# Optimization experiments

Hardware: AMD Instinct MI355X
Metric: run time of the kernel (lower is better)

The kernel has to match this reference:

```python
import jax, jax.numpy as jnp
import numpy as np

BATCH, SEQ, D_MODEL, D_STATE = 16, 1024, 512, 32
DT_MIN, DT_MAX, DT_FLOOR = 1e-3, 1e-1, 1e-4


def _init_ssm(key):
    k1, k2, k3, k4 = jax.random.split(key, 4)
    scale = 1.0 / np.sqrt(D_STATE)
    z = jax.random.normal(k1, (D_MODEL, D_STATE)) * scale
    A_log = -jnp.exp(z)  # A = exp(A_log) in (0,1)
    B = jax.random.normal(k2, (D_MODEL, D_STATE)) * scale
    C = jax.random.normal(k3, (D_MODEL, D_STATE)) * scale
    log_dt = jax.random.uniform(k4, (D_MODEL,)) * (np.log(DT_MAX) - np.log(DT_MIN)) + np.log(DT_MIN)
    log_dt = jnp.maximum(log_dt, np.log(DT_FLOOR))
    return A_log, B, C, log_dt


def setup_inputs() -> dict:
    key = jax.random.key(0)
    kx, khr, kbr = jax.random.split(key, 3)
    x = jax.random.normal(kx, (BATCH, SEQ, D_MODEL), dtype=jnp.float32)
    A_log_hr, B_hr, C_hr, log_dt_hr = _init_ssm(khr)
    A_log_br, B_br, C_br, log_dt_br = _init_ssm(kbr)
    return dict(
        x=x,
        A_log_hr=A_log_hr, B_hr=B_hr, C_hr=C_hr, log_dt_hr=log_dt_hr,
        A_log_br=A_log_br, B_br=B_br, C_br=C_br, log_dt_br=log_dt_br,
        weight_hr=jnp.ones((D_MODEL,), jnp.float32),
        weight_br=jnp.ones((D_MODEL,), jnp.float32),
    )


def _ssm(x, A_log, B, C, log_dt):
    # delta=None path: dt = exp(log_dt) * dt_scale(=1), time-invariant -> dA, dB are [d, n]
    dt = jnp.exp(log_dt)                 # [d]
    A = jnp.exp(A_log)                   # [d, n]
    dA = jnp.exp(dt[:, None] * A)        # [d, n]  (matches torch: exp(dt*exp(A_log)))
    dB = dt[:, None] * B                 # [d, n]
    b = x.shape[0]
    h0 = jnp.zeros((b, A.shape[0], A.shape[1]), x.dtype)  # [b, d, n]

    def step(h, xt):  # xt: [b, d]
        h = dA * h + dB * xt[:, :, None]
        y = jnp.einsum('bdn,dn->bd', h, C)
        return h, y

    _, ys = jax.lax.scan(step, h0, jnp.swapaxes(x, 0, 1))  # ys: [L, b, d]
    return jnp.swapaxes(ys, 0, 1)        # [b, L, d]


def reference(x, A_log_hr, B_hr, C_hr, log_dt_hr,
              A_log_br, B_br, C_br, log_dt_br,
              weight_hr, weight_br):
    x_hr = _ssm(x, A_log_hr, B_hr, C_hr, log_dt_hr) * weight_hr  # [b, L, d]
    x_br = _ssm(x, A_log_br, B_br, C_br, log_dt_br) * weight_br
    return (x_hr, x_br, x_hr + x_br)  # hr_enhanced, br_enhanced, combined
```

## Files before the change

kernel.cpp:

```cpp
#include <hip/hip_runtime.h>

#define BATCH 16
#define SEQ   1024
#define DM    512
#define NST   32
#define PF    8

#define PIN(v) asm volatile("" : "+v"(v))


__global__ __launch_bounds__(256) void ssm_setup(
    const float* __restrict__ Alog_hr, const float* __restrict__ B_hr,
    const float* __restrict__ C_hr,    const float* __restrict__ ldt_hr,
    const float* __restrict__ Alog_br, const float* __restrict__ B_br,
    const float* __restrict__ C_br,    const float* __restrict__ ldt_br,
    const float* __restrict__ w_hr,    const float* __restrict__ w_br,
    float* __restrict__ dA_tbl, float* __restrict__ Cw_tbl)
{
    int idx = blockIdx.x * blockDim.x + threadIdx.x;
    int d   = idx & (DM - 1);
    int n   = (idx >> 9) & (NST - 1);
    int ssm = idx >> 14;

    const float* Alog = ssm ? Alog_br : Alog_hr;
    const float* Bm   = ssm ? B_br    : B_hr;
    const float* Cm   = ssm ? C_br    : C_hr;
    const float* ldt  = ssm ? ldt_br  : ldt_hr;
    const float* w    = ssm ? w_br    : w_hr;

    float dt = expf(ldt[d]);
    float a  = expf(Alog[d * NST + n]);
    dA_tbl[idx] = expf(dt * a);
    Cw_tbl[idx] = Cm[d * NST + n] * Bm[d * NST + n] * dt * w[d];
}

__global__ __launch_bounds__(256) void ssm_pass1(
    const float* __restrict__ x,
    const float* __restrict__ Alog_hr, const float* __restrict__ ldt_hr,
    const float* __restrict__ Alog_br, const float* __restrict__ ldt_br,
    float* __restrict__ E, int nc, int cl)
{
    int tid  = threadIdx.x;
    int dlo  = tid & 127;
    int nh   = tid >> 7;
    int bid  = blockIdx.x;
    int dblk = bid & 3;
    int r    = bid >> 2;
    int ncm1 = nc - 1;
    int c    = r % ncm1;  r /= ncm1;
    int b    = r & (BATCH - 1);
    int ssm  = r >> 4;
    int d    = dblk * 128 + dlo;
    int n0   = nh * 16;

    const float* Alog = ssm ? Alog_br : Alog_hr;
    const float* ldt  = ssm ? ldt_br  : ldt_hr;

    float dt = expf(ldt[d]);
    float dA[16], g[16];
#pragma unroll
    for (int i = 0; i < 16; ++i) {
        dA[i] = expf(dt * expf(Alog[d * NST + n0 + i]));
        g[i]  = 0.f;
    }
#pragma unroll
    for (int i = 0; i < 16; ++i) PIN(dA[i]);

    const float* xp = x + ((size_t)b * SEQ + (size_t)c * cl) * DM + d;

    float xf[PF];
#pragma unroll
    for (int k = 0; k < PF; ++k) xf[k] = xp[(size_t)k * DM];
    const float* xq = xp + (size_t)PF * DM;

    int ntb = cl / PF;
    for (int t8 = 0; t8 < ntb - 1; ++t8) {
#pragma unroll
        for (int j = 0; j < PF; ++j) {
            float xv = xf[j];
            xf[j] = xq[(size_t)j * DM];
#pragma unroll
            for (int i = 0; i < 16; ++i) g[i] = fmaf(dA[i], g[i], xv);
        }
        xq += (size_t)PF * DM;
    }
#pragma unroll
    for (int j = 0; j < PF; ++j) {
        float xv = xf[j];
#pragma unroll
        for (int i = 0; i < 16; ++i) g[i] = fmaf(dA[i], g[i], xv);
    }

    float* sp = E + ((((size_t)ssm * BATCH + b) * nc + c) * NST + n0) * DM + d;
#pragma unroll
    for (int i = 0; i < 16; ++i) sp[(size_t)i * DM] = g[i];
}

__global__ __launch_bounds__(256) void ssm_pass2(
    const float* __restrict__ Alog_hr, const float* __restrict__ B_hr,
    const float* __restrict__ C_hr,    const float* __restrict__ ldt_hr,
    const float* __restrict__ Alog_br, const float* __restrict__ B_br,
    const float* __restrict__ C_br,    const float* __restrict__ ldt_br,
    const float* __restrict__ w_hr,    const float* __restrict__ w_br,
    float* __restrict__ E,
    float* __restrict__ dA_tbl, float* __restrict__ Cw_tbl,
    int nc, int cl)
{
    int idx = blockIdx.x * blockDim.x + threadIdx.x;
    int d   = idx & (DM - 1);
    int n   = (idx >> 9) & (NST - 1);
    int b   = (idx >> 14) & 15;
    int ssm = idx >> 18;

    const float* Alog = ssm ? Alog_br : Alog_hr;
    const float* ldt  = ssm ? ldt_br  : ldt_hr;

    float dt = expf(ldt[d]);
    float A  = expf(Alog[d * NST + n]);
    float p  = expf((float)cl * dt * A);

    if (b == 0) {
        const float* Bm = ssm ? B_br : B_hr;
        const float* Cm = ssm ? C_br : C_hr;
        const float* w  = ssm ? w_br : w_hr;
        int tix = (ssm * NST + n) * DM + d;
        dA_tbl[tix] = expf(dt * A);
        Cw_tbl[tix] = Cm[d * NST + n] * Bm[d * NST + n] * dt * w[d];
    }

    float* sp = E + ((((size_t)ssm * BATCH + b) * nc) * NST + n) * DM + d;
    size_t cstride = (size_t)NST * DM;

    float H = 0.f;
    for (int c = 0; c < nc; ++c) {
        float s = *sp;
        *sp = H;
        H = fmaf(p, H, s);
        sp += cstride;
    }
}

__global__ __launch_bounds__(128, 2) void ssm_pass3(
    const float* __restrict__ x,
    const float* __restrict__ dA_tbl, const float* __restrict__ Cw_tbl,
    const float* __restrict__ E,
    float* __restrict__ out_hr, float* __restrict__ out_br, float* __restrict__ out_cb,
    int nc, int cl)
{
    int tid  = threadIdx.x;
    int lane = tid & 63;
    int wid  = tid >> 6;
    int ssm  = lane >> 5;
    int dlo  = lane & 31;
    int bid  = blockIdx.x;
    int dblk = bid & 7;
    int r    = bid >> 3;
    int c    = r % nc;
    int b    = r / nc;
    int d    = dblk * 64 + wid * 32 + dlo;

    const float* dat = dA_tbl + (size_t)ssm * NST * DM + d;
    const float* cwt = Cw_tbl + (size_t)ssm * NST * DM + d;
    float dA[NST], Cw[NST];
#pragma unroll
    for (int n = 0; n < NST; ++n) {
        dA[n] = dat[(size_t)n * DM];
        Cw[n] = cwt[(size_t)n * DM];
    }
#pragma unroll
    for (int n = 0; n < NST; ++n) { PIN(dA[n]); PIN(Cw[n]); }

    float g[NST];
    if (c == 0) {
#pragma unroll
        for (int n = 0; n < NST; ++n) g[n] = 0.f;
    } else {
        const float* sp = E + ((((size_t)ssm * BATCH + b) * nc + c) * NST) * DM + d;
#pragma unroll
        for (int n = 0; n < NST; ++n) g[n] = sp[(size_t)n * DM];
    }

    size_t off = ((size_t)b * SEQ + (size_t)c * cl) * DM + d;
    const float* xp = x + off;
    float* po = (ssm ? out_br : out_hr) + off;
    float* oc = out_cb + off;

    float xf[PF];
#pragma unroll
    for (int k = 0; k < PF; ++k) xf[k] = xp[(size_t)k * DM];
    const float* xq = xp + (size_t)PF * DM;

#define BODY8(DOPF)                                                     \
    {                                                                   \
        float xc[PF];                                                   \
        _Pragma("unroll")                                               \
        for (int j = 0; j < PF; ++j) xc[j] = xf[j];                     \
        if (DOPF) {                             \
            _Pragma("unroll")                                           \
            for (int j = 0; j < PF; ++j) xf[j] = xq[(size_t)j * DM];    \
        }                                                               \
        float yv[PF], yw[PF];                                           \
        _Pragma("unroll")                                               \
        for (int j = 0; j < PF; ++j) {                                  \
            float xv = xc[j];                                           \
            float y0 = 0.f, y1 = 0.f, y2 = 0.f, y3 = 0.f;               \
            _Pragma("unroll")                                           \
            for (int n = 0; n < NST; n += 4) {                          \
                g[n]     = fmaf(dA[n],     g[n],     xv);               \
                g[n + 1] = fmaf(dA[n + 1], g[n + 1], xv);               \
                g[n + 2] = fmaf(dA[n + 2], g[n + 2], xv);               \
                g[n + 3] = fmaf(dA[n + 3], g[n + 3], xv);               \
                y0 = fmaf(Cw[n],     g[n],     y0);                     \
                y1 = fmaf(Cw[n + 1], g[n + 1], y1);                     \
                y2 = fmaf(Cw[n + 2], g[n + 2], y2);                     \
                y3 = fmaf(Cw[n + 3], g[n + 3], y3);                     \
            }                                                           \
            float y = (y0 + y1) + (y2 + y3);                            \
            yv[j] = y;                                                  \
            yw[j] = __shfl_xor(y, 32, 64);      \
            po[(size_t)j * DM] = y;                \
        }                                                               \
        if (ssm == 0) {                           \
            _Pragma("unroll")                                           \
            for (int j = 0; j < PF; ++j)                                \
                oc[(size_t)j * DM] = yv[j] + yw[j];                     \
        }                                                               \
        po += (size_t)PF * DM;  oc += (size_t)PF * DM;                  \
    }

    int ntb = cl / PF;
    for (int t8 = 0; t8 < ntb - 1; ++t8) {
        BODY8(1);
        xq += (size_t)PF * DM;
    }
    BODY8(0);
#undef BODY8
}

extern "C" void kernel_launch(void* const* d_in, const int* in_sizes, int n_in,
                              void* d_out, int out_size, void* d_ws, size_t ws_size,
                              hipStream_t stream)
{
    (void)in_sizes; (void)n_in; (void)out_size;

    const float* x       = (const float*)d_in[0];
    const float* Alog_hr = (const float*)d_in[1];
    const float* B_hr    = (const float*)d_in[2];
    const float* C_hr    = (const float*)d_in[3];
    const float* ldt_hr  = (const float*)d_in[4];
    const float* Alog_br = (const float*)d_in[5];
    const float* B_br    = (const float*)d_in[6];
    const float* C_br    = (const float*)d_in[7];
    const float* ldt_br  = (const float*)d_in[8];
    const float* w_hr    = (const float*)d_in[9];
    const float* w_br    = (const float*)d_in[10];

    float* out    = (float*)d_out;
    const size_t one = (size_t)BATCH * SEQ * DM;
    float* out_hr = out;
    float* out_br = out + one;
    float* out_cb = out + 2 * one;

    float* dA_tbl = (float*)d_ws;
    float* Cw_tbl = dA_tbl + (size_t)2 * NST * DM;
    float* E      = Cw_tbl + (size_t)2 * NST * DM;

    const size_t tbl_bytes = (size_t)4 * NST * DM * sizeof(float);
    int nc = 8;
    while (nc > 1 &&
           ws_size < tbl_bytes + (size_t)2 * BATCH * nc * NST * DM * sizeof(float))
        nc >>= 1;
    int cl = SEQ / nc;

    if (nc > 1) {
        int nblk1 = 2 * BATCH * (nc - 1) * 4;
        ssm_pass1<<<nblk1, 256, 0, stream>>>(x, Alog_hr, ldt_hr, Alog_br, ldt_br,
                                             E, nc, cl);
        int total2 = 2 * BATCH * NST * DM;
        ssm_pass2<<<total2 / 256, 256, 0, stream>>>(Alog_hr, B_hr, C_hr, ldt_hr,
                                                    Alog_br, B_br, C_br, ldt_br,
                                                    w_hr, w_br, E, dA_tbl, Cw_tbl,
                                                    nc, cl);
    } else {
        int total0 = 2 * NST * DM;
        ssm_setup<<<total0 / 256, 256, 0, stream>>>(Alog_hr, B_hr, C_hr, ldt_hr,
                                                    Alog_br, B_br, C_br, ldt_br,
                                                    w_hr, w_br, dA_tbl, Cw_tbl);
    }

    int nblk3 = BATCH * nc * 8;
    ssm_pass3<<<nblk3, 128, 0, stream>>>(x, dA_tbl, Cw_tbl, E,
                                         out_hr, out_br, out_cb, nc, cl);
}
```

Baseline: 68.08 us.

## Split state dimension across lane halves in pass3 to double parallelism

Result: slower. 74.91 us (+10.0%).

```diff
diff --git a/kernel.cpp b/kernel.cpp
--- a/kernel.cpp
+++ b/kernel.cpp
@@ -140,7 +140,7 @@
     }
 }
 
-__global__ __launch_bounds__(128, 2) void ssm_pass3(
+__global__ __launch_bounds__(128, 4) void ssm_pass3(
     const float* __restrict__ x,
     const float* __restrict__ dA_tbl, const float* __restrict__ Cw_tbl,
     const float* __restrict__ E,
@@ -151,39 +151,40 @@
     int lane = tid & 63;
     int wid  = tid >> 6;
     int ssm  = lane >> 5;
-    int dlo  = lane & 31;
+    int nh   = (lane >> 4) & 1;
+    int dlo  = lane & 15;
     int bid  = blockIdx.x;
-    int dblk = bid & 7;
-    int r    = bid >> 3;
+    int dblk = bid & 15;
+    int r    = bid >> 4;
     int c    = r % nc;
     int b    = r / nc;
-    int d    = dblk * 64 + wid * 32 + dlo;
-
-    const float* dat = dA_tbl + (size_t)ssm * NST * DM + d;
-    const float* cwt = Cw_tbl + (size_t)ssm * NST * DM + d;
-    float dA[NST], Cw[NST];
-#pragma unroll
-    for (int n = 0; n < NST; ++n) {
+    int d    = dblk * 32 + wid * 16 + dlo;
+    int n0   = nh * 16;
+
+    const float* dat = dA_tbl + ((size_t)ssm * NST + n0) * DM + d;
+    const float* cwt = Cw_tbl + ((size_t)ssm * NST + n0) * DM + d;
+    float dA[16], Cw[16];
+#pragma unroll
+    for (int n = 0; n < 16; ++n) {
         dA[n] = dat[(size_t)n * DM];
         Cw[n] = cwt[(size_t)n * DM];
     }
 #pragma unroll
-    for (int n = 0; n < NST; ++n) { PIN(dA[n]); PIN(Cw[n]); }
-
-    float g[NST];
+    for (int n = 0; n < 16; ++n) { PIN(dA[n]); PIN(Cw[n]); }
+
+    float g[16];
     if (c == 0) {
 #pragma unroll
-        for (int n = 0; n < NST; ++n) g[n] = 0.f;
+        for (int n = 0; n < 16; ++n) g[n] = 0.f;
     } else {
-        const float* sp = E + ((((size_t)ssm * BATCH + b) * nc + c) * NST) * DM + d;
-#pragma unroll
-        for (int n = 0; n < NST; ++n) g[n] = sp[(size_t)n * DM];
+        const float* sp = E + ((((size_t)ssm * BATCH + b) * nc + c) * NST + n0) * DM + d;
+#pragma unroll
+        for (int n = 0; n < 16; ++n) g[n] = sp[(size_t)n * DM];
     }
 
     size_t off = ((size_t)b * SEQ + (size_t)c * cl) * DM + d;
     const float* xp = x + off;
-    float* po = (ssm ? out_br : out_hr) + off;
-    float* oc = out_cb + off;
+    float* po = (nh ? out_cb : (ssm ? out_br : out_hr)) + off;
 
     float xf[PF];
 #pragma unroll
@@ -205,7 +206,7 @@
             float xv = xc[j];                                           \
             float y0 = 0.f, y1 = 0.f, y2 = 0.f, y3 = 0.f;               \
             _Pragma("unroll")                                           \
-            for (int n = 0; n < NST; n += 4) {                          \
+            for (int n = 0; n < 16; n += 4) {                           \
                 g[n]     = fmaf(dA[n],     g[n],     xv);               \
                 g[n + 1] = fmaf(dA[n + 1], g[n + 1], xv);               \
                 g[n + 2] = fmaf(dA[n + 2], g[n + 2], xv);               \
@@ -216,16 +217,16 @@
                 y3 = fmaf(Cw[n + 3], g[n + 3], y3);                     \
             }                                                           \
             float y = (y0 + y1) + (y2 + y3);                            \
-            yv[j] = y;                                                  \
-            yw[j] = __shfl_xor(y, 32, 64);      \
-            po[(size_t)j * DM] = y;                \
+            float yt = y + __shfl_xor(y, 16, 64);       \
+            yv[j] = yt;                                                 \
+            yw[j] = __shfl_xor(yt, 32, 64);     \
         }                                                               \
-        if (ssm == 0) {                           \
-            _Pragma("unroll")                                           \
-            for (int j = 0; j < PF; ++j)                                \
-                oc[(size_t)j * DM] = yv[j] + yw[j];                     \
+        _Pragma("unroll")                           \
+        for (int j = 0; j < PF; ++j) {                                  \
+            float val = nh ? (yv[j] + yw[j]) : yv[j];                   \
+            po[(size_t)j * DM] = val;                                   \
         }                                                               \
-        po += (size_t)PF * DM;  oc += (size_t)PF * DM;                  \
+        po += (size_t)PF * DM;                                          \
     }
 
     int ntb = cl / PF;
@@ -288,7 +289,7 @@
                                                     w_hr, w_br, dA_tbl, Cw_tbl);
     }
 
-    int nblk3 = BATCH * nc * 8;
+    int nblk3 = BATCH * nc * 16;
     ssm_pass3<<<nblk3, 128, 0, stream>>>(x, dA_tbl, Cw_tbl, E,
                                          out_hr, out_br, out_cb, nc, cl);
 }
```

## Fold chunk-carry scan into pass3 and table setup into pass1, removing pass2

Applied to the files above, without the earlier changes.

Result: faster. 65.91 us (-3.2%).

```diff
diff --git a/kernel.cpp b/kernel.cpp
--- a/kernel.cpp
+++ b/kernel.cpp
@@ -36,9 +36,14 @@
 
 __global__ __launch_bounds__(256) void ssm_pass1(
     const float* __restrict__ x,
-    const float* __restrict__ Alog_hr, const float* __restrict__ ldt_hr,
-    const float* __restrict__ Alog_br, const float* __restrict__ ldt_br,
-    float* __restrict__ E, int nc, int cl)
+    const float* __restrict__ Alog_hr, const float* __restrict__ B_hr,
+    const float* __restrict__ C_hr,    const float* __restrict__ ldt_hr,
+    const float* __restrict__ Alog_br, const float* __restrict__ B_br,
+    const float* __restrict__ C_br,    const float* __restrict__ ldt_br,
+    const float* __restrict__ w_hr,    const float* __restrict__ w_br,
+    float* __restrict__ E,
+    float* __restrict__ dA_tbl, float* __restrict__ Cw_tbl, float* __restrict__ p_tbl,
+    int nc, int cl)
 {
     int tid  = threadIdx.x;
     int dlo  = tid & 127;
@@ -63,6 +68,23 @@
         dA[i] = expf(dt * expf(Alog[d * NST + n0 + i]));
         g[i]  = 0.f;
     }
+
+    if (b == 0 && c == 0) {
+        const float* Bm = ssm ? B_br : B_hr;
+        const float* Cm = ssm ? C_br : C_hr;
+        const float* w  = ssm ? w_br : w_hr;
+        float wd = w[d];
+        float clf = (float)cl;
+#pragma unroll
+        for (int i = 0; i < 16; ++i) {
+            float a = expf(Alog[d * NST + n0 + i]);
+            int tix = (ssm * NST + n0 + i) * DM + d;
+            dA_tbl[tix] = dA[i];
+            p_tbl[tix]  = expf(clf * dt * a);
+            Cw_tbl[tix] = Cm[d * NST + n0 + i] * Bm[d * NST + n0 + i] * dt * wd;
+        }
+    }
+
 #pragma unroll
     for (int i = 0; i < 16; ++i) PIN(dA[i]);
 
@@ -96,53 +118,10 @@
     for (int i = 0; i < 16; ++i) sp[(size_t)i * DM] = g[i];
 }
 
-__global__ __launch_bounds__(256) void ssm_pass2(
-    const float* __restrict__ Alog_hr, const float* __restrict__ B_hr,
-    const float* __restrict__ C_hr,    const float* __restrict__ ldt_hr,
-    const float* __restrict__ Alog_br, const float* __restrict__ B_br,
-    const float* __restrict__ C_br,    const float* __restrict__ ldt_br,
-    const float* __restrict__ w_hr,    const float* __restrict__ w_br,
-    float* __restrict__ E,
-    float* __restrict__ dA_tbl, float* __restrict__ Cw_tbl,
-    int nc, int cl)
-{
-    int idx = blockIdx.x * blockDim.x + threadIdx.x;
-    int d   = idx & (DM - 1);
-    int n   = (idx >> 9) & (NST - 1);
-    int b   = (idx >> 14) & 15;
-    int ssm = idx >> 18;
-
-    const float* Alog = ssm ? Alog_br : Alog_hr;
-    const float* ldt  = ssm ? ldt_br  : ldt_hr;
-
-    float dt = expf(ldt[d]);
-    float A  = expf(Alog[d * NST + n]);
-    float p  = expf((float)cl * dt * A);
-
-    if (b == 0) {
-        const float* Bm = ssm ? B_br : B_hr;
-        const float* Cm = ssm ? C_br : C_hr;
-        const float* w  = ssm ? w_br : w_hr;
-        int tix = (ssm * NST + n) * DM + d;
-        dA_tbl[tix] = expf(dt * A);
-        Cw_tbl[tix] = Cm[d * NST + n] * Bm[d * NST + n] * dt * w[d];
-    }
-
-    float* sp = E + ((((size_t)ssm * BATCH + b) * nc) * NST + n) * DM + d;
-    size_t cstride = (size_t)NST * DM;
-
-    float H = 0.f;
-    for (int c = 0; c < nc; ++c) {
-        float s = *sp;
-        *sp = H;
-        H = fmaf(p, H, s);
-        sp += cstride;
-    }
-}
-
 __global__ __launch_bounds__(128, 2) void ssm_pass3(
     const float* __restrict__ x,
     const float* __restrict__ dA_tbl, const float* __restrict__ Cw_tbl,
+    const float* __restrict__ p_tbl,
     const float* __restrict__ E,
     float* __restrict__ out_hr, float* __restrict__ out_br, float* __restrict__ out_cb,
     int nc, int cl)
@@ -159,6 +138,26 @@
     int b    = r / nc;
     int d    = dblk * 64 + wid * 32 + dlo;
 
+    float g[NST];
+#pragma unroll
+    for (int n = 0; n < NST; ++n) g[n] = 0.f;
+    if (c > 0) {
+        const float* pt = p_tbl + (size_t)ssm * NST * DM + d;
+        float p[NST];
+#pragma unroll
+        for (int n = 0; n < NST; ++n) p[n] = pt[(size_t)n * DM];
+        const size_t slab = (size_t)NST * DM;
+        const float* ep = E + (((size_t)ssm * BATCH + b) * nc) * slab + d;
+        for (int cc = 0; cc < c; ++cc) {
+            float e[NST];
+#pragma unroll
+            for (int n = 0; n < NST; ++n) e[n] = ep[(size_t)n * DM];
+#pragma unroll
+            for (int n = 0; n < NST; ++n) g[n] = fmaf(p[n], g[n], e[n]);
+            ep += slab;
+        }
+    }
+
     const float* dat = dA_tbl + (size_t)ssm * NST * DM + d;
     const float* cwt = Cw_tbl + (size_t)ssm * NST * DM + d;
     float dA[NST], Cw[NST];
@@ -169,16 +168,6 @@
     }
 #pragma unroll
     for (int n = 0; n < NST; ++n) { PIN(dA[n]); PIN(Cw[n]); }
-
-    float g[NST];
-    if (c == 0) {
-#pragma unroll
-        for (int n = 0; n < NST; ++n) g[n] = 0.f;
-    } else {
-        const float* sp = E + ((((size_t)ssm * BATCH + b) * nc + c) * NST) * DM + d;
-#pragma unroll
-        for (int n = 0; n < NST; ++n) g[n] = sp[(size_t)n * DM];
-    }
 
     size_t off = ((size_t)b * SEQ + (size_t)c * cl) * DM + d;
     const float* xp = x + off;
@@ -263,9 +252,10 @@
 
     float* dA_tbl = (float*)d_ws;
     float* Cw_tbl = dA_tbl + (size_t)2 * NST * DM;
-    float* E      = Cw_tbl + (size_t)2 * NST * DM;
-
-    const size_t tbl_bytes = (size_t)4 * NST * DM * sizeof(float);
+    float* p_tbl  = Cw_tbl + (size_t)2 * NST * DM;
+    float* E      = p_tbl  + (size_t)2 * NST * DM;
+
+    const size_t tbl_bytes = (size_t)6 * NST * DM * sizeof(float);
     int nc = 8;
     while (nc > 1 &&
            ws_size < tbl_bytes + (size_t)2 * BATCH * nc * NST * DM * sizeof(float))
@@ -274,13 +264,11 @@
 
     if (nc > 1) {
         int nblk1 = 2 * BATCH * (nc - 1) * 4;
-        ssm_pass1<<<nblk1, 256, 0, stream>>>(x, Alog_hr, ldt_hr, Alog_br, ldt_br,
-                                             E, nc, cl);
-        int total2 = 2 * BATCH * NST * DM;
-        ssm_pass2<<<total2 / 256, 256, 0, stream>>>(Alog_hr, B_hr, C_hr, ldt_hr,
-                                                    Alog_br, B_br, C_br, ldt_br,
-                                                    w_hr, w_br, E, dA_tbl, Cw_tbl,
-                                                    nc, cl);
+        ssm_pass1<<<nblk1, 256, 0, stream>>>(x,
+                                             Alog_hr, B_hr, C_hr, ldt_hr,
+                                             Alog_br, B_br, C_br, ldt_br,
+                                             w_hr, w_br,
+                                             E, dA_tbl, Cw_tbl, p_tbl, nc, cl);
     } else {
         int total0 = 2 * NST * DM;
         ssm_setup<<<total0 / 256, 256, 0, stream>>>(Alog_hr, B_hr, C_hr, ldt_hr,
@@ -289,6 +277,6 @@
     }
 
     int nblk3 = BATCH * nc * 8;
-    ssm_pass3<<<nblk3, 128, 0, stream>>>(x, dA_tbl, Cw_tbl, E,
+    ssm_pass3<<<nblk3, 128, 0, stream>>>(x, dA_tbl, Cw_tbl, p_tbl, E,
                                          out_hr, out_br, out_cb, nc, cl);
 }
```
